# Performance work log

Measured on AMD Instinct MI355X. Metric: run time of the kernel, lower is better.

## Reference

```python
import jax, jax.numpy as jnp
import numpy as np

N_HEADS = 16
N_DIM = 1024
H_DIM = N_DIM // N_HEADS


def setup_inputs() -> dict:
    key = jax.random.key(0)
    ks = jax.random.split(key, 9)
    s = 1.0 / np.sqrt(N_DIM)
    x = jax.random.normal(ks[0], (4, 2048, N_DIM), dtype=jnp.float32)
    Wq = jax.random.uniform(ks[1], (N_DIM, N_DIM), jnp.float32, -s, s)
    bq = jax.random.uniform(ks[2], (N_DIM,), jnp.float32, -s, s)
    Wk = jax.random.uniform(ks[3], (N_DIM, N_DIM), jnp.float32, -s, s)
    bk = jax.random.uniform(ks[4], (N_DIM,), jnp.float32, -s, s)
    Wv = jax.random.uniform(ks[5], (N_DIM, N_DIM), jnp.float32, -s, s)
    bv = jax.random.uniform(ks[6], (N_DIM,), jnp.float32, -s, s)
    Wp = jax.random.uniform(ks[7], (N_DIM, N_DIM), jnp.float32, -s, s)
    bp = jax.random.uniform(ks[8], (N_DIM,), jnp.float32, -s, s)
    return {"x": x, "Wq": Wq, "bq": bq, "Wk": Wk, "bk": bk,
            "Wv": Wv, "bv": bv, "Wp": Wp, "bp": bp}


def _split_heads(y):
    # [b, t, (nh*hd)] -> [nh, b, t, hd]
    b, t, _ = y.shape
    return y.reshape(b, t, N_HEADS, H_DIM).transpose(2, 0, 1, 3)


def reference(x, Wq, bq, Wk, bk, Wv, bv, Wp, bp):
    q = _split_heads(x @ Wq.T + bq)
    k = _split_heads(x @ Wk.T + bk)
    v = _split_heads(x @ Wv.T + bv)
    # NOTE: original module applies NO 1/sqrt(d) scaling
    energies = jnp.einsum('hbqd,hbkd->hbqk', q, k)
    attn = jax.nn.softmax(energies, axis=-1)  # dropout disabled (eval)
    out = jnp.einsum('hbqk,hbkd->hbqd', attn, v)
    # [nh, b, t, hd] -> [b, t, nh*hd]
    b, t = out.shape[1], out.shape[2]
    out = out.transpose(1, 2, 0, 3).reshape(b, t, N_DIM)
    return out @ Wp.T + bp
```

## Files before the change

kernel.cpp:

```cpp
#include <hip/hip_runtime.h>
#include <hip/hip_bf16.h>


typedef short short8 __attribute__((ext_vector_type(8)));
typedef float float4v __attribute__((ext_vector_type(4)));

#define MFMA16(a, b, c) __builtin_amdgcn_mfma_f32_16x16x32_bf16((a), (b), (c), 0, 0, 0)
#define LOG2E 1.4426950408889634f

#define B_SZ 4
#define T_SZ 2048
#define D_SZ 1024
#define NH 16
#define HD 64
#define M_SZ (B_SZ * T_SZ)

__device__ __forceinline__ unsigned short f2bf(float f) {
  unsigned int u = __float_as_uint(f);
  u += 0x7fffu + ((u >> 16) & 1u);
  return (unsigned short)(u >> 16);
}

__device__ __forceinline__ float fexp2(float x) {
#if __has_builtin(__builtin_amdgcn_exp2f)
  return __builtin_amdgcn_exp2f(x);
#else
  return exp2f(x);
#endif
}

__device__ __forceinline__ void gl_lds16(const unsigned short* g, unsigned short* l) {
  __builtin_amdgcn_global_load_lds(
      (const __attribute__((address_space(1))) unsigned int*)g,
      (__attribute__((address_space(3))) unsigned int*)l, 16, 0, 0);
}

__global__ __launch_bounds__(256) void cvt_kernel(const float* __restrict__ in,
                                                  unsigned short* __restrict__ out,
                                                  float scale, long n) {
  long i = ((long)blockIdx.x * 256 + threadIdx.x) * 4;
  if (i >= n) return;
  float4 v = *(const float4*)(in + i);
  uint2 o;
  o.x = (unsigned)f2bf(v.x * scale) | ((unsigned)f2bf(v.y * scale) << 16);
  o.y = (unsigned)f2bf(v.z * scale) | ((unsigned)f2bf(v.w * scale) << 16);
  *(uint2*)(out + i) = o;
}

__global__ __launch_bounds__(256) void cvt_w(const float* __restrict__ w0,
                                             const float* __restrict__ w1,
                                             const float* __restrict__ w2,
                                             const float* __restrict__ w3,
                                             unsigned short* __restrict__ out, long per) {
  long i = ((long)blockIdx.x * 256 + threadIdx.x) * 4;
  int which = (int)(i / per);
  const float* src = which == 0 ? w0 : which == 1 ? w1 : which == 2 ? w2 : w3;
  float scale = which == 0 ? LOG2E : 1.0f;
  long j = i - (long)which * per;
  float4 v = *(const float4*)(src + j);
  uint2 o;
  o.x = (unsigned)f2bf(v.x * scale) | ((unsigned)f2bf(v.y * scale) << 16);
  o.y = (unsigned)f2bf(v.z * scale) | ((unsigned)f2bf(v.w * scale) << 16);
  *(uint2*)(out + i) = o;
}

__global__ __launch_bounds__(256) void cvt_bias(const float* __restrict__ b0,
                                                const float* __restrict__ b1,
                                                const float* __restrict__ b2,
                                                float* __restrict__ out) {
  int i = blockIdx.x * 256 + threadIdx.x;
  float v;
  if (i < 1024) v = b0[i] * LOG2E;
  else if (i < 2048) v = b1[i - 1024];
  else v = b2[i - 2048];
  out[i] = v;
}

__global__ __launch_bounds__(256, 3) void gemm_qkv(const unsigned short* __restrict__ A,
                                                   const unsigned short* __restrict__ W,
                                                   const float* __restrict__ bias,
                                                   unsigned short* __restrict__ Qb,
                                                   unsigned short* __restrict__ Kb,
                                                   unsigned short* __restrict__ Vt) {
  __shared__ __align__(16) unsigned short smem[17408];
  unsigned short* As = smem;
  unsigned short* Bs = smem + 8192;
  unsigned short* Ct = smem;
  const int tid = threadIdx.x;
  const int wave = tid >> 6, lane = tid & 63;
  const int q = lane >> 4, ln = lane & 15;
  const int wm = (wave >> 1) * 64, wn = (wave & 1) * 64;
  const long m0 = (long)blockIdx.y * 128;
  const long n0 = (long)blockIdx.x * 128;
  const int srow = lane >> 3, scol = (lane & 7) * 8;
  const int K = D_SZ;

  float4v acc[4][4] = {};

  for (int k0 = 0; k0 < K; k0 += 64) {
    for (int t = 0; t < 4; ++t) {
      int seg = wave * 4 + t;
      int row = seg * 8 + srow;
      gl_lds16(A + (m0 + row) * (long)K + k0 + scol, As + seg * 512);
      gl_lds16(W + (n0 + row) * (long)K + k0 + scol, Bs + seg * 512);
    }
    __syncthreads();
    for (int ks = 0; ks < 2; ++ks) {
      short8 af[4], bf[4];
      for (int i = 0; i < 4; ++i)
        af[i] = *(const short8*)(As + (wm + i * 16 + ln) * 64 + ks * 32 + q * 8);
      for (int j = 0; j < 4; ++j)
        bf[j] = *(const short8*)(Bs + (wn + j * 16 + ln) * 64 + ks * 32 + q * 8);
      for (int i = 0; i < 4; ++i)
        for (int j = 0; j < 4; ++j)
          acc[i][j] = MFMA16(af[i], bf[j], acc[i][j]);
    }
    __syncthreads();
  }

  if ((int)n0 < 2048) {
    unsigned short* dst = (int)n0 < 1024 ? Qb : Kb;
    int coff = (int)n0 < 1024 ? 0 : 1024;
    for (int i = 0; i < 4; ++i) {
      long rowb = m0 + wm + i * 16 + q * 4;
      for (int j = 0; j < 4; ++j) {
        long col = n0 + wn + j * 16 + ln;
        float bv = bias[col];
        for (int r = 0; r < 4; ++r)
          dst[(rowb + r) * (long)D_SZ + col - coff] = f2bf(acc[i][j][r] + bv);
      }
    }
  } else {
    for (int i = 0; i < 4; ++i)
      for (int j = 0; j < 4; ++j) {
        int col_l = wn + j * 16 + ln;
        float bv = bias[n0 + col_l];
        __hip_bfloat162 lo =
            __float22bfloat162_rn(make_float2(acc[i][j][0] + bv, acc[i][j][1] + bv));
        __hip_bfloat162 hi =
            __float22bfloat162_rn(make_float2(acc[i][j][2] + bv, acc[i][j][3] + bv));
        uint2 w;
        w.x = *(unsigned*)&lo;
        w.y = *(unsigned*)&hi;
        *(uint2*)(Ct + col_l * 136 + wm + i * 16 + q * 4) = w;
      }
    __syncthreads();
    for (int it = 0; it < 8; ++it) {
      int idx = tid + it * 256;
      int c = idx >> 4, rb = idx & 15;
      uint4 v = *(const uint4*)(Ct + c * 136 + rb * 8);
      *(uint4*)(Vt + (n0 - 2048 + c) * (long)M_SZ + m0 + rb * 8) = v;
    }
  }
}

__global__ __launch_bounds__(256, 3) void gemm_proj(const unsigned short* __restrict__ A,
                                                    const unsigned short* __restrict__ W,
                                                    const float* __restrict__ bias,
                                                    float* __restrict__ Cf) {
  __shared__ __align__(16) unsigned short As[128 * 64];
  __shared__ __align__(16) unsigned short Bs[128 * 64];
  const int tid = threadIdx.x;
  const int wave = tid >> 6, lane = tid & 63;
  const int q = lane >> 4, ln = lane & 15;
  const int wm = (wave >> 1) * 64, wn = (wave & 1) * 64;
  const long m0 = (long)blockIdx.y * 128;
  const long n0 = (long)blockIdx.x * 128;
  const int srow = lane >> 3, scol = (lane & 7) * 8;
  const int K = D_SZ;

  float4v acc[4][4] = {};
  for (int k0 = 0; k0 < K; k0 += 64) {
    for (int t = 0; t < 4; ++t) {
      int seg = wave * 4 + t;
      int row = seg * 8 + srow;
      gl_lds16(A + (m0 + row) * (long)K + k0 + scol, As + seg * 512);
      gl_lds16(W + (n0 + row) * (long)K + k0 + scol, Bs + seg * 512);
    }
    __syncthreads();
    for (int ks = 0; ks < 2; ++ks) {
      short8 af[4], bf[4];
      for (int i = 0; i < 4; ++i)
        af[i] = *(const short8*)(As + (wm + i * 16 + ln) * 64 + ks * 32 + q * 8);
      for (int j = 0; j < 4; ++j)
        bf[j] = *(const short8*)(Bs + (wn + j * 16 + ln) * 64 + ks * 32 + q * 8);
      for (int i = 0; i < 4; ++i)
        for (int j = 0; j < 4; ++j)
          acc[i][j] = MFMA16(af[i], bf[j], acc[i][j]);
    }
    __syncthreads();
  }
  for (int i = 0; i < 4; ++i) {
    long rowb = m0 + wm + i * 16 + q * 4;
    for (int j = 0; j < 4; ++j) {
      long col = n0 + wn + j * 16 + ln;
      float bv = bias[col];
      for (int r = 0; r < 4; ++r)
        Cf[(rowb + r) * (long)D_SZ + col] = acc[i][j][r] + bv;
    }
  }
}

__global__ __launch_bounds__(512, 4) void attn_kernel(const unsigned short* __restrict__ Qb,
                                                      const unsigned short* __restrict__ Kb,
                                                      const unsigned short* __restrict__ Vt,
                                                      unsigned short* __restrict__ Ob) {
  __shared__ __align__(16) unsigned short KV[16384];
  __shared__ __align__(16) unsigned short Pp[10240];

  const int tid = threadIdx.x;
  const int wave = tid >> 6, lane = tid & 63;
  const int q = lane >> 4, ln = lane & 15;
  const int l7 = lane & 7, l3 = lane >> 3;
  const int qt = blockIdx.x, h = blockIdx.y, b = blockIdx.z;

  const long baseQ = ((long)b * T_SZ + qt * 256) * D_SZ + h * HD;
  const long baseK = (long)b * T_SZ * D_SZ + h * HD;
  const long baseV = (long)h * HD * M_SZ + (long)b * T_SZ;
  const int cs = ((l7 ^ l3) * 8);

  short8 qf[2][2];
  for (int i = 0; i < 2; ++i)
    for (int ks = 0; ks < 2; ++ks)
      qf[i][ks] = *(const short8*)(Qb + baseQ + (long)(wave * 32 + i * 16 + ln) * D_SZ +
                                   ks * 32 + q * 8);

  float4v o[2][4] = {};
  float lp[2] = {};
  unsigned short* Ppw = Pp + wave * (32 * 40);
  const int swz = (ln & 7) * 8;

#define STAGE(kt_, base_)                                                                \
  {                                                                                      \
    int row = wave * 8 + l3;                                                             \
    gl_lds16(Kb + baseK + (long)((kt_)*64 + row) * D_SZ + cs, (base_) + wave * 512);     \
    gl_lds16(Vt + baseV + (long)row * M_SZ + (kt_)*64 + cs, (base_) + 4096 + wave * 512);\
  }

  STAGE(0, KV)

  for (int kt = 0; kt < 32; ++kt) {
    unsigned short* cur = KV + (kt & 1) * 8192;
    unsigned short* nxt = KV + ((kt & 1) ^ 1) * 8192;
    __syncthreads();
    if (kt < 31) { STAGE(kt + 1, nxt) }

    short8 kf[4][2];
    for (int c = 0; c < 4; ++c)
      for (int ks = 0; ks < 2; ++ks)
        kf[c][ks] = *(const short8*)(cur + (c * 16 + ln) * 64 + ((ks * 32 + q * 8) ^ swz));
    float4v s[4][2];
    for (int c = 0; c < 4; ++c)
      for (int i = 0; i < 2; ++i) {
        float4v z = {};
        z = MFMA16(kf[c][0], qf[i][0], z);
        z = MFMA16(kf[c][1], qf[i][1], z);
        s[c][i] = z;
      }

    for (int ks = 0; ks < 2; ++ks) {
      for (int i = 0; i < 2; ++i)
        for (int cl = 0; cl < 2; ++cl) {
          int c = 2 * ks + cl;
          float p0 = fexp2(s[c][i][0]);
          float p1 = fexp2(s[c][i][1]);
          float p2 = fexp2(s[c][i][2]);
          float p3 = fexp2(s[c][i][3]);
          lp[i] += (p0 + p1) + (p2 + p3);
          __hip_bfloat162 lo = __float22bfloat162_rn(make_float2(p0, p1));
          __hip_bfloat162 hi = __float22bfloat162_rn(make_float2(p2, p3));
          uint2 w;
          w.x = *(unsigned*)&lo;
          w.y = *(unsigned*)&hi;
          *(uint2*)(Ppw + (i * 16 + ln) * 40 + cl * 16 + q * 4) = w;
        }
      short8 vf[4];
      for (int j = 0; j < 4; ++j)
        vf[j] = *(const short8*)(cur + 4096 + (j * 16 + ln) * 64 + ((ks * 32 + q * 8) ^ swz));
      short8 pf[2];
      for (int i = 0; i < 2; ++i)
        pf[i] = *(const short8*)(Ppw + (i * 16 + ln) * 40 + q * 8);
      for (int i = 0; i < 2; ++i)
        for (int j = 0; j < 4; ++j)
          o[i][j] = MFMA16(pf[i], vf[j], o[i][j]);
    }
  }

  for (int i = 0; i < 2; ++i) {
    float l = lp[i];
    l += __shfl_xor(l, 16, 64);
    l += __shfl_xor(l, 32, 64);
    float inv = 1.f / l;
    for (int r = 0; r < 4; ++r) {
      int src = (lane & 48) | (q * 4 + r);
      float invr = __shfl(inv, src, 64);
      int row = qt * 256 + wave * 32 + i * 16 + q * 4 + r;
      long base = ((long)b * T_SZ + row) * D_SZ + h * HD;
      for (int j = 0; j < 4; ++j)
        Ob[base + j * 16 + ln] = f2bf(o[i][j][r] * invr);
    }
  }
#undef STAGE
}

extern "C" void kernel_launch(void* const* d_in, const int* in_sizes, int n_in,
                              void* d_out, int out_size, void* d_ws, size_t ws_size,
                              hipStream_t stream) {
  const float* x = (const float*)d_in[0];
  const float* Wq = (const float*)d_in[1];
  const float* bq = (const float*)d_in[2];
  const float* Wk = (const float*)d_in[3];
  const float* bk = (const float*)d_in[4];
  const float* Wv = (const float*)d_in[5];
  const float* bv = (const float*)d_in[6];
  const float* Wp = (const float*)d_in[7];
  const float* bp = (const float*)d_in[8];
  float* out = (float*)d_out;

  const long MX = (long)M_SZ * D_SZ;
  const long MW = (long)D_SZ * D_SZ;
  unsigned short* ws = (unsigned short*)d_ws;
  unsigned short* xb = ws;
  unsigned short* Wcat = xb + MX;
  float* bcat = (float*)(Wcat + 4 * MW);
  unsigned short* Qb = (unsigned short*)(bcat + 3072);
  unsigned short* Kb = Qb + MX;
  unsigned short* Vtb = Kb + MX;
  unsigned short* Ob = Vtb + MX;

  cvt_kernel<<<(int)(MX / 1024), 256, 0, stream>>>(x, xb, 1.0f, MX);
  cvt_w<<<(int)(4 * MW / 1024), 256, 0, stream>>>(Wq, Wk, Wv, Wp, Wcat, MW);
  cvt_bias<<<12, 256, 0, stream>>>(bq, bk, bv, bcat);

  dim3 gq(3072 / 128, M_SZ / 128);
  gemm_qkv<<<gq, 256, 0, stream>>>(xb, Wcat, bcat, Qb, Kb, Vtb);

  dim3 ag(T_SZ / 256, NH, B_SZ);
  attn_kernel<<<ag, 512, 0, stream>>>(Qb, Kb, Vtb, Ob);

  dim3 gp(D_SZ / 128, M_SZ / 128);
  gemm_proj<<<gp, 256, 0, stream>>>(Ob, Wcat + 3 * MW, bp, out);
}
```

Baseline: 277.8 us.

## Rewrite QKV GEMM as 256x256 double-buffered pipelined kernel with swizzled LDS

Replaces the 128x128 single-buffered QKV GEMM with a 256x256 tile, 512-thread kernel that double-buffers A and B in LDS. Global-to-LDS loads for the next k-steps are interleaved with MFMA phases, using explicit waitcnt, barriers and setprio. LDS rows are XOR-swizzled to avoid bank conflicts. The V-transpose epilogue now writes directly to global memory instead of staging through LDS. The kernel uses 128KB of LDS and many accumulator registers, which limits occupancy, and the direct V stores are narrower and more scattered.

```diff
diff --git a/kernel.cpp b/kernel.cpp
--- a/kernel.cpp
+++ b/kernel.cpp
@@ -76,80 +76,162 @@
   out[i] = v;
 }
 
-__global__ __launch_bounds__(256, 3) void gemm_qkv(const unsigned short* __restrict__ A,
+__device__ __forceinline__ short8 ldf(const unsigned short* b, int row, int col) {
+  return *(const short8*)(b + row * 64 + (col ^ ((row & 7) * 8)));
+}
+
+__device__ __forceinline__ void ld_a(const unsigned short* bA, int rbase, int ln, int q,
+                                     short8 f[4][2]) {
+#pragma unroll
+  for (int m = 0; m < 4; ++m)
+#pragma unroll
+    for (int ks = 0; ks < 2; ++ks)
+      f[m][ks] = ldf(bA, rbase + m * 16 + ln, ks * 32 + q * 8);
+}
+
+__device__ __forceinline__ void ld_b(const unsigned short* bB, int rbase, int ln, int q,
+                                     short8 f[2][2]) {
+#pragma unroll
+  for (int n = 0; n < 2; ++n)
+#pragma unroll
+    for (int ks = 0; ks < 2; ++ks)
+      f[n][ks] = ldf(bB, rbase + n * 16 + ln, ks * 32 + q * 8);
+}
+
+__device__ __forceinline__ void mf_q(float4v (&acc)[8][4], const short8 af[4][2],
+                                     const short8 bf[2][2], int mo, int no) {
+#pragma unroll
+  for (int m = 0; m < 4; ++m)
+#pragma unroll
+    for (int n = 0; n < 2; ++n) {
+      float4v c = acc[m + mo][n + no];
+      c = MFMA16(af[m][0], bf[n][0], c);
+      c = MFMA16(af[m][1], bf[n][1], c);
+      acc[m + mo][n + no] = c;
+    }
+}
+
+__device__ __forceinline__ void stg_half(const unsigned short* __restrict__ g, long row0,
+                                         int kcol, unsigned short* dst, int wave, int l3,
+                                         int l7) {
+  const int cs = (l7 ^ l3) * 8;
+#pragma unroll
+  for (int c = 0; c < 2; ++c)
+    gl_lds16(g + (row0 + c * 64 + wave * 8 + l3) * (long)D_SZ + kcol + cs,
+             dst + c * 4096 + wave * 512);
+}
+
+#define PH_PRE                                            \
+  do {                                                    \
+    __builtin_amdgcn_s_barrier();                         \
+    asm volatile("s_waitcnt lgkmcnt(0)" ::: "memory");    \
+    __builtin_amdgcn_s_setprio(1);                        \
+  } while (0)
+#define PH_POST                                           \
+  do {                                                    \
+    __builtin_amdgcn_s_setprio(0);                        \
+    __builtin_amdgcn_s_barrier();                         \
+  } while (0)
+
+__global__ __launch_bounds__(512, 2) void gemm_qkv(const unsigned short* __restrict__ A,
                                                    const unsigned short* __restrict__ W,
                                                    const float* __restrict__ bias,
                                                    unsigned short* __restrict__ Qb,
                                                    unsigned short* __restrict__ Kb,
                                                    unsigned short* __restrict__ Vt) {
-  __shared__ __align__(16) unsigned short smem[17408];
-  unsigned short* As = smem;
-  unsigned short* Bs = smem + 8192;
-  unsigned short* Ct = smem;
+  __shared__ __align__(16) unsigned short sm[65536];
+  unsigned short* sA0 = sm;
+  unsigned short* sB0 = sm + 16384;
+  unsigned short* sA1 = sm + 32768;
+  unsigned short* sB1 = sm + 49152;
   const int tid = threadIdx.x;
   const int wave = tid >> 6, lane = tid & 63;
   const int q = lane >> 4, ln = lane & 15;
-  const int wm = (wave >> 1) * 64, wn = (wave & 1) * 64;
-  const long m0 = (long)blockIdx.y * 128;
-  const long n0 = (long)blockIdx.x * 128;
-  const int srow = lane >> 3, scol = (lane & 7) * 8;
-  const int K = D_SZ;
-
-  float4v acc[4][4] = {};
-
-  for (int k0 = 0; k0 < K; k0 += 64) {
-    for (int t = 0; t < 4; ++t) {
-      int seg = wave * 4 + t;
-      int row = seg * 8 + srow;
-      gl_lds16(A + (m0 + row) * (long)K + k0 + scol, As + seg * 512);
-      gl_lds16(W + (n0 + row) * (long)K + k0 + scol, Bs + seg * 512);
-    }
-    __syncthreads();
-    for (int ks = 0; ks < 2; ++ks) {
-      short8 af[4], bf[4];
-      for (int i = 0; i < 4; ++i)
-        af[i] = *(const short8*)(As + (wm + i * 16 + ln) * 64 + ks * 32 + q * 8);
-      for (int j = 0; j < 4; ++j)
-        bf[j] = *(const short8*)(Bs + (wn + j * 16 + ln) * 64 + ks * 32 + q * 8);
-      for (int i = 0; i < 4; ++i)
-        for (int j = 0; j < 4; ++j)
-          acc[i][j] = MFMA16(af[i], bf[j], acc[i][j]);
-    }
-    __syncthreads();
-  }
+  const int l7 = lane & 7, l3 = lane >> 3;
+  const int wm = (wave >> 2) * 128, wn = (wave & 3) * 64;
+  const long m0 = (long)blockIdx.y * 256;
+  const long n0 = (long)blockIdx.x * 256;
+
+  float4v acc[8][4] = {};
+  short8 aL[4][2], aH[4][2], bL[2][2], bH[2][2];
+
+  stg_half(A, m0, 0, sA0, wave, l3, l7);
+  stg_half(A, m0 + 128, 0, sA0 + 8192, wave, l3, l7);
+  stg_half(W, n0, 0, sB0, wave, l3, l7);
+  stg_half(W, n0 + 128, 0, sB0 + 8192, wave, l3, l7);
+  stg_half(W, n0, 64, sB1, wave, l3, l7);
+  stg_half(W, n0 + 128, 64, sB1 + 8192, wave, l3, l7);
+  __syncthreads();
+
+#pragma unroll 1
+  for (int it = 0; it < 8; ++it) {
+    const int T = it * 2;
+    const int k1 = (T + 1) * 64;
+    const int k2 = (T + 2 < 16 ? T + 2 : 15) * 64;
+    const int k3 = (T + 3 < 16 ? T + 3 : 15) * 64;
+
+    ld_a(sA0, wm, ln, q, aL);
+    ld_b(sB0, wn, ln, q, bL);
+    stg_half(A, m0, k1, sA1, wave, l3, l7);
+    PH_PRE; mf_q(acc, aL, bL, 0, 0); PH_POST;
+    ld_b(sB0, wn + 32, ln, q, bH);
+    stg_half(A, m0 + 128, k1, sA1 + 8192, wave, l3, l7);
+    PH_PRE; mf_q(acc, aL, bH, 0, 2); PH_POST;
+    ld_a(sA0, wm + 64, ln, q, aH);
+    stg_half(W, n0, k2, sB0, wave, l3, l7);
+    PH_PRE; mf_q(acc, aH, bL, 4, 0); PH_POST;
+    stg_half(W, n0 + 128, k2, sB0 + 8192, wave, l3, l7);
+    asm volatile("s_waitcnt vmcnt(4)" ::: "memory");
+    PH_PRE; mf_q(acc, aH, bH, 4, 2); PH_POST;
+
+    ld_a(sA1, wm, ln, q, aL);
+    ld_b(sB1, wn, ln, q, bL);
+    stg_half(A, m0, k2, sA0, wave, l3, l7);
+    PH_PRE; mf_q(acc, aL, bL, 0, 0); PH_POST;
+    ld_b(sB1, wn + 32, ln, q, bH);
+    stg_half(A, m0 + 128, k2, sA0 + 8192, wave, l3, l7);
+    PH_PRE; mf_q(acc, aL, bH, 0, 2); PH_POST;
+    ld_a(sA1, wm + 64, ln, q, aH);
+    stg_half(W, n0, k3, sB1, wave, l3, l7);
+    PH_PRE; mf_q(acc, aH, bL, 4, 0); PH_POST;
+    stg_half(W, n0 + 128, k3, sB1 + 8192, wave, l3, l7);
+    asm volatile("s_waitcnt vmcnt(4)" ::: "memory");
+    PH_PRE; mf_q(acc, aH, bH, 4, 2); PH_POST;
+  }
+  asm volatile("s_waitcnt vmcnt(0)" ::: "memory");
 
   if ((int)n0 < 2048) {
     unsigned short* dst = (int)n0 < 1024 ? Qb : Kb;
-    int coff = (int)n0 < 1024 ? 0 : 1024;
-    for (int i = 0; i < 4; ++i) {
+    const int coff = (int)n0 < 1024 ? 0 : 1024;
+#pragma unroll
+    for (int i = 0; i < 8; ++i) {
       long rowb = m0 + wm + i * 16 + q * 4;
+#pragma unroll
       for (int j = 0; j < 4; ++j) {
         long col = n0 + wn + j * 16 + ln;
         float bv = bias[col];
+#pragma unroll
         for (int r = 0; r < 4; ++r)
           dst[(rowb + r) * (long)D_SZ + col - coff] = f2bf(acc[i][j][r] + bv);
       }
     }
   } else {
-    for (int i = 0; i < 4; ++i)
+#pragma unroll
+    for (int i = 0; i < 8; ++i) {
+      long rowb = m0 + wm + i * 16 + q * 4;
+#pragma unroll
       for (int j = 0; j < 4; ++j) {
-        int col_l = wn + j * 16 + ln;
-        float bv = bias[n0 + col_l];
-        __hip_bfloat162 lo =
-            __float22bfloat162_rn(make_float2(acc[i][j][0] + bv, acc[i][j][1] + bv));
-        __hip_bfloat162 hi =
-            __float22bfloat162_rn(make_float2(acc[i][j][2] + bv, acc[i][j][3] + bv));
-        uint2 w;
-        w.x = *(unsigned*)&lo;
-        w.y = *(unsigned*)&hi;
-        *(uint2*)(Ct + col_l * 136 + wm + i * 16 + q * 4) = w;
+        int cl = wn + j * 16 + ln;
+        float bv = bias[n0 + cl];
+        unsigned p01 = (unsigned)f2bf(acc[i][j][0] + bv) |
+                       ((unsigned)f2bf(acc[i][j][1] + bv) << 16);
+        unsigned p23 = (unsigned)f2bf(acc[i][j][2] + bv) |
+                       ((unsigned)f2bf(acc[i][j][3] + bv) << 16);
+        uint2 wv;
+        wv.x = p01;
+        wv.y = p23;
+        *(uint2*)(Vt + ((long)(n0 - 2048) + cl) * (long)M_SZ + rowb) = wv;
       }
-    __syncthreads();
-    for (int it = 0; it < 8; ++it) {
-      int idx = tid + it * 256;
-      int c = idx >> 4, rb = idx & 15;
-      uint4 v = *(const uint4*)(Ct + c * 136 + rb * 8);
-      *(uint4*)(Vt + (n0 - 2048 + c) * (long)M_SZ + m0 + rb * 8) = v;
     }
   }
 }
@@ -332,8 +414,8 @@
   cvt_w<<<(int)(4 * MW / 1024), 256, 0, stream>>>(Wq, Wk, Wv, Wp, Wcat, MW);
   cvt_bias<<<12, 256, 0, stream>>>(bq, bk, bv, bcat);
 
-  dim3 gq(3072 / 128, M_SZ / 128);
-  gemm_qkv<<<gq, 256, 0, stream>>>(xb, Wcat, bcat, Qb, Kb, Vtb);
+  dim3 gq(3072 / 256, M_SZ / 256);
+  gemm_qkv<<<gq, 512, 0, stream>>>(xb, Wcat, bcat, Qb, Kb, Vtb);
 
   dim3 ag(T_SZ / 256, NH, B_SZ);
   attn_kernel<<<ag, 512, 0, stream>>>(Qb, Kb, Vtb, Ob);
```

New measurement: 286.8 us. +3.2%, slower.

## Merge conversion kernels and shrink GEMM tiles to 128x64 for more blocks

Applied to the files above, without the earlier changes.

Folds the three fp32-to-bf16 conversion kernels (activations, weights, biases) into one launch with block-range dispatch, which removes two kernel launches. Both GEMMs (QKV and projection) go from 128x128 tiles to 128x64 tiles, with each wave owning a 32x64 sub-tile. Launch bounds rise to 4 blocks per CU and LDS use is cut. This doubles the block count so the 256 CUs are filled more evenly, in exchange for less operand reuse per tile and more global/LDS traffic per FLOP.

```diff
diff --git a/kernel.cpp b/kernel.cpp
--- a/kernel.cpp
+++ b/kernel.cpp
@@ -14,6 +14,7 @@
 #define NH 16
 #define HD 64
 #define M_SZ (B_SZ * T_SZ)
+#define MW_SZ (D_SZ * D_SZ)
 
 __device__ __forceinline__ unsigned short f2bf(float f) {
   unsigned int u = __float_as_uint(f);
@@ -35,83 +36,91 @@
       (__attribute__((address_space(3))) unsigned int*)l, 16, 0, 0);
 }
 
-__global__ __launch_bounds__(256) void cvt_kernel(const float* __restrict__ in,
-                                                  unsigned short* __restrict__ out,
-                                                  float scale, long n) {
-  long i = ((long)blockIdx.x * 256 + threadIdx.x) * 4;
-  if (i >= n) return;
-  float4 v = *(const float4*)(in + i);
-  uint2 o;
-  o.x = (unsigned)f2bf(v.x * scale) | ((unsigned)f2bf(v.y * scale) << 16);
-  o.y = (unsigned)f2bf(v.z * scale) | ((unsigned)f2bf(v.w * scale) << 16);
-  *(uint2*)(out + i) = o;
-}
-
-__global__ __launch_bounds__(256) void cvt_w(const float* __restrict__ w0,
-                                             const float* __restrict__ w1,
-                                             const float* __restrict__ w2,
-                                             const float* __restrict__ w3,
-                                             unsigned short* __restrict__ out, long per) {
-  long i = ((long)blockIdx.x * 256 + threadIdx.x) * 4;
-  int which = (int)(i / per);
-  const float* src = which == 0 ? w0 : which == 1 ? w1 : which == 2 ? w2 : w3;
-  float scale = which == 0 ? LOG2E : 1.0f;
-  long j = i - (long)which * per;
-  float4 v = *(const float4*)(src + j);
-  uint2 o;
-  o.x = (unsigned)f2bf(v.x * scale) | ((unsigned)f2bf(v.y * scale) << 16);
-  o.y = (unsigned)f2bf(v.z * scale) | ((unsigned)f2bf(v.w * scale) << 16);
-  *(uint2*)(out + i) = o;
-}
-
-__global__ __launch_bounds__(256) void cvt_bias(const float* __restrict__ b0,
-                                                const float* __restrict__ b1,
-                                                const float* __restrict__ b2,
-                                                float* __restrict__ out) {
-  int i = blockIdx.x * 256 + threadIdx.x;
-  float v;
-  if (i < 1024) v = b0[i] * LOG2E;
-  else if (i < 2048) v = b1[i - 1024];
-  else v = b2[i - 2048];
-  out[i] = v;
-}
-
-__global__ __launch_bounds__(256, 3) void gemm_qkv(const unsigned short* __restrict__ A,
+__global__ __launch_bounds__(256) void cvt_all(const float* __restrict__ x,
+                                               const float* __restrict__ w0,
+                                               const float* __restrict__ w1,
+                                               const float* __restrict__ w2,
+                                               const float* __restrict__ w3,
+                                               const float* __restrict__ b0,
+                                               const float* __restrict__ b1,
+                                               const float* __restrict__ b2,
+                                               unsigned short* __restrict__ xb,
+                                               unsigned short* __restrict__ wout,
+                                               float* __restrict__ bout) {
+  const long blk = blockIdx.x;
+  if (blk < 8192) {
+    long i = (blk * 256 + threadIdx.x) * 4;
+    float4 v = *(const float4*)(x + i);
+    uint2 o;
+    o.x = (unsigned)f2bf(v.x) | ((unsigned)f2bf(v.y) << 16);
+    o.y = (unsigned)f2bf(v.z) | ((unsigned)f2bf(v.w) << 16);
+    *(uint2*)(xb + i) = o;
+  } else if (blk < 12288) {
+    long i = ((blk - 8192) * 256 + threadIdx.x) * 4;
+    int which = (int)(i >> 20);
+    const float* src = which == 0 ? w0 : which == 1 ? w1 : which == 2 ? w2 : w3;
+    float scale = which == 0 ? LOG2E : 1.0f;
+    long j = i - (long)which * MW_SZ;
+    float4 v = *(const float4*)(src + j);
+    uint2 o;
+    o.x = (unsigned)f2bf(v.x * scale) | ((unsigned)f2bf(v.y * scale) << 16);
+    o.y = (unsigned)f2bf(v.z * scale) | ((unsigned)f2bf(v.w * scale) << 16);
+    *(uint2*)(wout + i) = o;
+  } else {
+    int i = (int)((blk - 12288) * 256 + threadIdx.x) * 4;
+    float4 v;
+    if (i < 1024) {
+      v = *(const float4*)(b0 + i);
+      v.x *= LOG2E; v.y *= LOG2E; v.z *= LOG2E; v.w *= LOG2E;
+    } else if (i < 2048) {
+      v = *(const float4*)(b1 + (i - 1024));
+    } else {
+      v = *(const float4*)(b2 + (i - 2048));
+    }
+    *(float4*)(bout + i) = v;
+  }
+}
+
+__global__ __launch_bounds__(256, 4) void gemm_qkv(const unsigned short* __restrict__ A,
                                                    const unsigned short* __restrict__ W,
                                                    const float* __restrict__ bias,
                                                    unsigned short* __restrict__ Qb,
                                                    unsigned short* __restrict__ Kb,
                                                    unsigned short* __restrict__ Vt) {
-  __shared__ __align__(16) unsigned short smem[17408];
+  __shared__ __align__(16) unsigned short smem[12288];
   unsigned short* As = smem;
   unsigned short* Bs = smem + 8192;
   unsigned short* Ct = smem;
   const int tid = threadIdx.x;
   const int wave = tid >> 6, lane = tid & 63;
   const int q = lane >> 4, ln = lane & 15;
-  const int wm = (wave >> 1) * 64, wn = (wave & 1) * 64;
+  const int wm = wave * 32;
   const long m0 = (long)blockIdx.y * 128;
-  const long n0 = (long)blockIdx.x * 128;
+  const long n0 = (long)blockIdx.x * 64;
   const int srow = lane >> 3, scol = (lane & 7) * 8;
   const int K = D_SZ;
 
-  float4v acc[4][4] = {};
+  float4v acc[2][4] = {};
 
   for (int k0 = 0; k0 < K; k0 += 64) {
     for (int t = 0; t < 4; ++t) {
       int seg = wave * 4 + t;
       int row = seg * 8 + srow;
       gl_lds16(A + (m0 + row) * (long)K + k0 + scol, As + seg * 512);
+    }
+    for (int t = 0; t < 2; ++t) {
+      int seg = wave * 2 + t;
+      int row = seg * 8 + srow;
       gl_lds16(W + (n0 + row) * (long)K + k0 + scol, Bs + seg * 512);
     }
     __syncthreads();
     for (int ks = 0; ks < 2; ++ks) {
-      short8 af[4], bf[4];
-      for (int i = 0; i < 4; ++i)
+      short8 af[2], bf[4];
+      for (int i = 0; i < 2; ++i)
         af[i] = *(const short8*)(As + (wm + i * 16 + ln) * 64 + ks * 32 + q * 8);
       for (int j = 0; j < 4; ++j)
-        bf[j] = *(const short8*)(Bs + (wn + j * 16 + ln) * 64 + ks * 32 + q * 8);
-      for (int i = 0; i < 4; ++i)
+        bf[j] = *(const short8*)(Bs + (j * 16 + ln) * 64 + ks * 32 + q * 8);
+      for (int i = 0; i < 2; ++i)
         for (int j = 0; j < 4; ++j)
           acc[i][j] = MFMA16(af[i], bf[j], acc[i][j]);
     }
@@ -121,19 +130,19 @@
   if ((int)n0 < 2048) {
     unsigned short* dst = (int)n0 < 1024 ? Qb : Kb;
     int coff = (int)n0 < 1024 ? 0 : 1024;
-    for (int i = 0; i < 4; ++i) {
+    for (int i = 0; i < 2; ++i) {
       long rowb = m0 + wm + i * 16 + q * 4;
       for (int j = 0; j < 4; ++j) {
-        long col = n0 + wn + j * 16 + ln;
+        long col = n0 + j * 16 + ln;
         float bv = bias[col];
         for (int r = 0; r < 4; ++r)
           dst[(rowb + r) * (long)D_SZ + col - coff] = f2bf(acc[i][j][r] + bv);
       }
     }
   } else {
-    for (int i = 0; i < 4; ++i)
+    for (int i = 0; i < 2; ++i)
       for (int j = 0; j < 4; ++j) {
-        int col_l = wn + j * 16 + ln;
+        int col_l = j * 16 + ln;
         float bv = bias[n0 + col_l];
         __hip_bfloat162 lo =
             __float22bfloat162_rn(make_float2(acc[i][j][0] + bv, acc[i][j][1] + bv));
@@ -145,7 +154,7 @@
         *(uint2*)(Ct + col_l * 136 + wm + i * 16 + q * 4) = w;
       }
     __syncthreads();
-    for (int it = 0; it < 8; ++it) {
+    for (int it = 0; it < 4; ++it) {
       int idx = tid + it * 256;
       int c = idx >> 4, rb = idx & 15;
       uint4 v = *(const uint4*)(Ct + c * 136 + rb * 8);
@@ -154,46 +163,50 @@
   }
 }
 
-__global__ __launch_bounds__(256, 3) void gemm_proj(const unsigned short* __restrict__ A,
+__global__ __launch_bounds__(256, 4) void gemm_proj(const unsigned short* __restrict__ A,
                                                     const unsigned short* __restrict__ W,
                                                     const float* __restrict__ bias,
                                                     float* __restrict__ Cf) {
   __shared__ __align__(16) unsigned short As[128 * 64];
-  __shared__ __align__(16) unsigned short Bs[128 * 64];
+  __shared__ __align__(16) unsigned short Bs[64 * 64];
   const int tid = threadIdx.x;
   const int wave = tid >> 6, lane = tid & 63;
   const int q = lane >> 4, ln = lane & 15;
-  const int wm = (wave >> 1) * 64, wn = (wave & 1) * 64;
+  const int wm = wave * 32;
   const long m0 = (long)blockIdx.y * 128;
-  const long n0 = (long)blockIdx.x * 128;
+  const long n0 = (long)blockIdx.x * 64;
   const int srow = lane >> 3, scol = (lane & 7) * 8;
   const int K = D_SZ;
 
-  float4v acc[4][4] = {};
+  float4v acc[2][4] = {};
   for (int k0 = 0; k0 < K; k0 += 64) {
     for (int t = 0; t < 4; ++t) {
       int seg = wave * 4 + t;
       int row = seg * 8 + srow;
       gl_lds16(A + (m0 + row) * (long)K + k0 + scol, As + seg * 512);
+    }
+    for (int t = 0; t < 2; ++t) {
+      int seg = wave * 2 + t;
+      int row = seg * 8 + srow;
       gl_lds16(W + (n0 + row) * (long)K + k0 + scol, Bs + seg * 512);
     }
     __syncthreads();
     for (int ks = 0; ks < 2; ++ks) {
-      short8 af[4], bf[4];
-      for (int i = 0; i < 4; ++i)
+      short8 af[2], bf[4];
+      for (int i = 0; i < 2; ++i)
         af[i] = *(const short8*)(As + (wm + i * 16 + ln) * 64 + ks * 32 + q * 8);
       for (int j = 0; j < 4; ++j)
-        bf[j] = *(const short8*)(Bs + (wn + j * 16 + ln) * 64 + ks * 32 + q * 8);
-      for (int i = 0; i < 4; ++i)
+        bf[j] = *(const short8*)(Bs + (j * 16 + ln) * 64 + ks * 32 + q * 8);
+      for (int i = 0; i < 2; ++i)
         for (int j = 0; j < 4; ++j)
           acc[i][j] = MFMA16(af[i], bf[j], acc[i][j]);
     }
     __syncthreads();
   }
-  for (int i = 0; i < 4; ++i) {
+  for (int i = 0; i < 2; ++i) {
     long rowb = m0 + wm + i * 16 + q * 4;
     for (int j = 0; j < 4; ++j) {
-      long col = n0 + wn + j * 16 + ln;
+      long col = n0 + j * 16 + ln;
       float bv = bias[col];
       for (int r = 0; r < 4; ++r)
         Cf[(rowb + r) * (long)D_SZ + col] = acc[i][j][r] + bv;
@@ -318,7 +331,7 @@
   float* out = (float*)d_out;
 
   const long MX = (long)M_SZ * D_SZ;
-  const long MW = (long)D_SZ * D_SZ;
+  const long MW = (long)MW_SZ;
   unsigned short* ws = (unsigned short*)d_ws;
   unsigned short* xb = ws;
   unsigned short* Wcat = xb + MX;
@@ -328,16 +341,14 @@
   unsigned short* Vtb = Kb + MX;
   unsigned short* Ob = Vtb + MX;
 
-  cvt_kernel<<<(int)(MX / 1024), 256, 0, stream>>>(x, xb, 1.0f, MX);
-  cvt_w<<<(int)(4 * MW / 1024), 256, 0, stream>>>(Wq, Wk, Wv, Wp, Wcat, MW);
-  cvt_bias<<<12, 256, 0, stream>>>(bq, bk, bv, bcat);
-
-  dim3 gq(3072 / 128, M_SZ / 128);
+  cvt_all<<<12291, 256, 0, stream>>>(x, Wq, Wk, Wv, Wp, bq, bk, bv, xb, Wcat, bcat);
+
+  dim3 gq(3072 / 64, M_SZ / 128);
   gemm_qkv<<<gq, 256, 0, stream>>>(xb, Wcat, bcat, Qb, Kb, Vtb);
 
   dim3 ag(T_SZ / 256, NH, B_SZ);
   attn_kernel<<<ag, 512, 0, stream>>>(Qb, Kb, Vtb, Ob);
 
-  dim3 gp(D_SZ / 128, M_SZ / 128);
+  dim3 gp(D_SZ / 64, M_SZ / 128);
   gemm_proj<<<gp, 256, 0, stream>>>(Ob, Wcat + 3 * MW, bp, out);
 }
```

New measurement: 290.2 us. +4.5%, slower.
